# Kernel optimization log

Hardware: AMD Instinct MI355X
Metric: run time of the kernel (lower is better)

Reference implementation:

```python
import jax, jax.numpy as jnp
import numpy as np

P = 113          # modulus; eq_token = P, vocab = P + 1
D_MODEL = 1024
D_MLP = 4096
BATCH = 16384


def setup_inputs() -> dict:
    key = jax.random.key(0)
    ks = jax.random.split(key, 9)
    return {
        "a": jax.random.randint(ks[0], (BATCH,), 0, P, dtype=jnp.int64 if jax.config.jax_enable_x64 else jnp.int32),
        "b": jax.random.randint(ks[1], (BATCH,), 0, P, dtype=jnp.int64 if jax.config.jax_enable_x64 else jnp.int32),
        "token_embed": jax.random.normal(ks[2], (P + 1, D_MODEL), dtype=jnp.float32),
        "pos_embed": jax.random.normal(ks[3], (3, D_MODEL), dtype=jnp.float32),
        "W_in_w": jax.random.normal(ks[4], (D_MLP, D_MODEL), dtype=jnp.float32) * (1.0 / np.sqrt(D_MODEL)),
        "W_in_b": jax.random.normal(ks[5], (D_MLP,), dtype=jnp.float32) * 0.02,
        "W_out_w": jax.random.normal(ks[6], (D_MODEL, D_MLP), dtype=jnp.float32) * (1.0 / np.sqrt(D_MLP)),
        "W_out_b": jax.random.normal(ks[7], (D_MODEL,), dtype=jnp.float32) * 0.02,
        "unembed_w": jax.random.normal(ks[8], (P, D_MODEL), dtype=jnp.float32) * (1.0 / np.sqrt(D_MODEL)),
    }


def reference(a, b, token_embed, pos_embed, W_in_w, W_in_b, W_out_w, W_out_b, unembed_w):
    # tokens: (batch, 3) = [a, b, eq]
    eq = jnp.full_like(a, P)
    tokens = jnp.stack([a, b, eq], axis=1)
    # embed + positional: (batch, 3, d_model)
    x = token_embed[tokens] + pos_embed[None, :, :]
    # FNet-style mixing: FFT over seq (axis 1), then over d_model (axis 2), real part
    wave = jnp.fft.fft(jnp.fft.fft(x, axis=1), axis=2).real.astype(x.dtype)
    x = x + wave
    # MLP with residual
    h = jax.nn.relu(jnp.einsum('bsd,md->bsm', x, W_in_w) + W_in_b)
    x = x + jnp.einsum('bsm,dm->bsd', h, W_out_w) + W_out_b
    # unembed only the '=' position (index 2)
    logits = jnp.einsum('bd,vd->bv', x[:, 2, :], unembed_w)
    return logits
```

## Files before the change

### kernel.cpp

```cpp
#include <hip/hip_runtime.h>

typedef __attribute__((ext_vector_type(4))) float f32x4;
typedef __attribute__((ext_vector_type(8))) short short8;

#define PMOD 113
#define DM 1024
#define DMLP 4096
#define NBATCH 16384
#define SQRT3_2 0.86602540378443865f
#define CSTEP 6.1359231515425649e-3f
#define LTSTRIDE (12800 * 128)
#define NZ 8

__device__ __forceinline__ short f2bf(float x) {
    unsigned int u = __builtin_bit_cast(unsigned int, x);
    u += 0x7FFFu + ((u >> 16) & 1u);
    return (short)(u >> 16);
}
__device__ __forceinline__ float bf2f(short s) {
    return __builtin_bit_cast(float, (unsigned int)(unsigned short)s << 16);
}
__device__ __forceinline__ void cvt16(const float* p, short8& o0, short8& o1) {
    #pragma unroll
    for (int c4 = 0; c4 < 4; ++c4) {
        f32x4 v = *(const f32x4*)(p + c4 * 4);
        #pragma unroll
        for (int e = 0; e < 4; ++e) {
            short s = f2bf(v[e]);
            if (c4 < 2) o0[c4 * 4 + e] = s; else o1[(c4 - 2) * 4 + e] = s;
        }
    }
}

__global__ __launch_bounds__(256) void k_prep(
    unsigned short* __restrict__ Fb, unsigned short* __restrict__ V2b,
    unsigned short* __restrict__ Wob,
    const float* __restrict__ E, const float* __restrict__ pos,
    const float* __restrict__ Wo)
{
    __shared__ float smem[64 * 65];
    const int blk = blockIdx.x, tid = threadIdx.x;

    if (blk < 1024) {
        const int f = blk;
        for (int k = tid; k < DM; k += 256) {
            float v;
            if (k <= 512) v = cosf((float)((f * k) & 1023) * CSTEP);
            else          v = sinf((float)((f * (k - 512)) & 1023) * CSTEP);
            Fb[f * DM + k] = (unsigned short)f2bf(v);
        }
    } else if (blk < 1252) {
        const int t = blk - 1024;
        if (t >= 226) {
            for (int k = tid; k < DM; k += 256) V2b[t * DM + k] = 0;
            return;
        }
        float* vc = smem;
        float* vs = smem + 1024;
        if (t < PMOD) {
            const float* e = E + t * DM;
            const float* e2 = E + PMOD * DM;
            for (int d = tid; d < DM; d += 256) {
                float e2v = e2[d] + pos[2 * DM + d];
                vc[d] = e[d] + pos[d] - 0.5f * pos[DM + d] - 0.5f * e2v;
                vs[d] = SQRT3_2 * (pos[DM + d] - e2v);
            }
        } else {
            const float* e = E + (t - PMOD) * DM;
            for (int d = tid; d < DM; d += 256) {
                float x = e[d];
                vc[d] = -0.5f * x;
                vs[d] = SQRT3_2 * x;
            }
        }
        __syncthreads();
        for (int k = tid; k < DM; k += 256) {
            float o;
            if (k == 0)        o = vc[0];
            else if (k < 512)  o = vc[k] + vc[1024 - k];
            else if (k == 512) o = vc[512];
            else               o = vs[k - 512] - vs[1536 - k];
            V2b[t * DM + k] = (unsigned short)f2bf(o);
        }
    } else {
        const int idx = blk - 1252;
        const int m0 = (idx & 63) * 64;
        const int d0 = (idx >> 6) * 64;
        float (*tile)[65] = (float(*)[65])smem;
        #pragma unroll
        for (int it = 0; it < 16; ++it) {
            int i2 = tid + it * 256;
            int r = i2 >> 6, c = i2 & 63;
            tile[c][r] = Wo[(d0 + r) * DMLP + m0 + c];
        }
        __syncthreads();
        #pragma unroll
        for (int it = 0; it < 16; ++it) {
            int i2 = tid + it * 256;
            int r = i2 >> 6, c = i2 & 63;
            Wob[(m0 + r) * DM + d0 + c] = (unsigned short)f2bf(tile[r][c]);
        }
    }
}

template<int MODE>
__device__ __forceinline__ void mfma_body(
    int n0, int row0,
    unsigned short* __restrict__ C1, float* __restrict__ C2,
    const void* __restrict__ Av, const void* __restrict__ B1v,
    const float* __restrict__ B2, const float* __restrict__ bias,
    const float* __restrict__ E, const float* __restrict__ pos,
    const float* __restrict__ bo, short* sA, short* sB)
{
    const int tid = threadIdx.x;
    const int sr = tid >> 2, sq = (tid & 3) * 16;
    const int lane = tid & 63, w = tid >> 6;
    const int wr = w >> 1, wc = w & 1;
    const int lr = lane & 15, lg = lane >> 4;

    const unsigned short* Ab = nullptr; const float* Af = nullptr;
    {
        int r = row0 + sr;
        if (MODE == 2) { if (r < PMOD) Af = (const float*)Av + r * DM; }
        else           { if (r < 228)  Ab = (const unsigned short*)Av + r * DM; }
    }
    const unsigned short* Bb = nullptr; const float* Bf = nullptr;
    {
        int n = n0 + sr;
        if (MODE == 1) {
            if (n < 4096) Bf = (const float*)B1v + n * DM;
            else if (n - 4096 < PMOD) Bf = B2 + (n - 4096) * DM;
        } else {
            Bb = (const unsigned short*)B1v + n * DM;
        }
    }

    f32x4 acc[2][2];
    #pragma unroll
    for (int i = 0; i < 2; ++i)
        #pragma unroll
        for (int j = 0; j < 2; ++j) acc[i][j] = 0.f;

    for (int k0 = 0; k0 < DM; k0 += 64) {
        short8 a0, a1, b0, b1;
        if (MODE == 2) {
            if (Af) cvt16(Af + k0 + sq, a0, a1);
            else { a0 = 0; a1 = 0; }
        } else {
            if (Ab) { a0 = ((const short8*)(Ab + k0 + sq))[0];
                      a1 = ((const short8*)(Ab + k0 + sq))[1]; }
            else { a0 = 0; a1 = 0; }
        }
        if (MODE == 1) {
            if (Bf) cvt16(Bf + k0 + sq, b0, b1);
            else { b0 = 0; b1 = 0; }
        } else {
            b0 = ((const short8*)(Bb + k0 + sq))[0];
            b1 = ((const short8*)(Bb + k0 + sq))[1];
        }
        if (k0) __syncthreads();
        *(short8*)&sA[sr * 72 + sq] = a0;
        *(short8*)&sA[sr * 72 + sq + 8] = a1;
        *(short8*)&sB[sr * 72 + sq] = b0;
        *(short8*)&sB[sr * 72 + sq + 8] = b1;
        __syncthreads();

        #pragma unroll
        for (int ks = 0; ks < 2; ++ks) {
            short8 af[2], bfr[2];
            #pragma unroll
            for (int i = 0; i < 2; ++i)
                af[i] = *(const short8*)&sA[(wr * 32 + i * 16 + lr) * 72 + ks * 32 + lg * 8];
            #pragma unroll
            for (int j = 0; j < 2; ++j)
                bfr[j] = *(const short8*)&sB[(wc * 32 + j * 16 + lr) * 72 + ks * 32 + lg * 8];
            #pragma unroll
            for (int i = 0; i < 2; ++i)
                #pragma unroll
                for (int j = 0; j < 2; ++j)
                    acc[i][j] = __builtin_amdgcn_mfma_f32_16x16x32_bf16(af[i], bfr[j], acc[i][j], 0, 0, 0);
        }
    }

    #pragma unroll
    for (int i = 0; i < 2; ++i) {
        #pragma unroll
        for (int q = 0; q < 4; ++q) {
            int r = row0 + wr * 32 + i * 16 + lg * 4 + q;
            #pragma unroll
            for (int j = 0; j < 2; ++j) {
                int cg = n0 + wc * 32 + j * 16 + lr;
                float v = acc[i][j][q];
                if (MODE == 0) {
                    if (r < 228) {
                        if (r < PMOD) v += E[PMOD * DM + cg] + pos[2 * DM + cg];
                        if (r == 227) v += bo[cg];
                        C1[r * DM + cg] = (unsigned short)f2bf(v);
                    }
                } else if (MODE == 1) {
                    if (r < 228) {
                        if (n0 < 4096) {
                            if (r < PMOD) v += bias[cg];
                            C1[r * DMLP + cg] = (unsigned short)f2bf(v);
                        } else {
                            C2[r * 128 + cg - 4096] = v;
                        }
                    }
                } else {
                    if (r < 128) C1[r * DMLP + cg] = (unsigned short)f2bf(v);
                }
            }
        }
    }
}

__global__ __launch_bounds__(256) void k_m02(
    unsigned short* __restrict__ Tb, unsigned short* __restrict__ Mb,
    const unsigned short* __restrict__ V2b, const unsigned short* __restrict__ Fb,
    const float* __restrict__ U, const unsigned short* __restrict__ Wob,
    const float* __restrict__ E, const float* __restrict__ pos,
    const float* __restrict__ bo)
{
    __shared__ short sA[64 * 72];
    __shared__ short sB[64 * 72];
    const int blk = blockIdx.x;
    if (blk < 64) {
        mfma_body<0>((blk & 15) * 64, (blk >> 4) * 64, Tb, nullptr, V2b, Fb,
                     nullptr, nullptr, E, pos, bo, sA, sB);
    } else {
        int i = blk - 64;
        mfma_body<2>((i & 63) * 64, (i >> 6) * 64, Mb, nullptr, U, Wob,
                     nullptr, nullptr, nullptr, nullptr, nullptr, sA, sB);
    }
}

__global__ __launch_bounds__(256) void k_m1(
    unsigned short* __restrict__ Hb, float* __restrict__ L,
    const unsigned short* __restrict__ Tb, const float* __restrict__ Wi,
    const float* __restrict__ U, const float* __restrict__ bi)
{
    __shared__ short sA[64 * 72];
    __shared__ short sB[64 * 72];
    mfma_body<1>(blockIdx.x * 64, blockIdx.y * 64, Hb, L, Tb, Wi, U, bi,
                 nullptr, nullptr, nullptr, sA, sB);
}

__global__ __launch_bounds__(512) void k_pair_gemm(
    unsigned short* __restrict__ LTp,
    const unsigned short* __restrict__ Hb,
    const unsigned short* __restrict__ Mb,
    const float* __restrict__ L)
{
    __shared__ short mB[128 * 512];
    __shared__ short hA[2][64 * 72];

    const int tid = threadIdx.x;
    const int z = blockIdx.x;
    const int g = blockIdx.y;
    const int kbeg = z * 512;
    const bool slice0 = (z == 0);
    unsigned short* outp = LTp + (size_t)z * LTSTRIDE;

    const int lane = tid & 63, w = tid >> 6;
    const int wr = w >> 2, wc = w & 3;
    const int lr = lane & 15, lg = lane >> 4;
    const int sr = tid >> 3, sq8 = (tid & 7) * 8;

    {
        const int l8 = lane * 8;
        #pragma unroll
        for (int r = 0; r < 16; ++r) {
            int v = w * 16 + r;
            short8 d = *(const short8*)(Mb + v * DMLP + kbeg + l8);
            *(short8*)&mB[v * 512 + (l8 ^ ((v & 7) << 3))] = d;
        }
    }

    for (int u = g; u < 226; u += 32) {
        const int a = u >> 1;
        const int b0 = (u & 1) * 64;
        const int brow = b0 + sr;
        const int brc = brow < PMOD ? brow : PMOD - 1;
        const unsigned short* pA = Hb + a * DMLP + kbeg + sq8;
        const unsigned short* pB = Hb + (PMOD + brc) * DMLP + kbeg + sq8;

        f32x4 acc[2][2];
        #pragma unroll
        for (int i = 0; i < 2; ++i)
            #pragma unroll
            for (int j = 0; j < 2; ++j) acc[i][j] = 0.f;

        short8 ra = *(const short8*)pA;
        short8 rb = *(const short8*)pB;

        #pragma unroll
        for (int t = 0; t < 8; ++t) {
            short8 ran = ra, rbn = rb;
            if (t < 7) {
                ran = *(const short8*)(pA + (t + 1) * 64);
                rbn = *(const short8*)(pB + (t + 1) * 64);
            }
            short8 uu;
            #pragma unroll
            for (int e = 0; e < 8; ++e)
                uu[e] = f2bf(fmaxf(bf2f(ra[e]) + bf2f(rb[e]), 0.f));
            *(short8*)&hA[t & 1][sr * 72 + sq8] = uu;
            __syncthreads();

            #pragma unroll
            for (int ks = 0; ks < 2; ++ks) {
                short8 af[2], bfr[2];
                #pragma unroll
                for (int i = 0; i < 2; ++i)
                    af[i] = *(const short8*)&hA[t & 1][(wr * 32 + i * 16 + lr) * 72 + ks * 32 + lg * 8];
                #pragma unroll
                for (int j = 0; j < 2; ++j) {
                    int v = wc * 32 + j * 16 + lr;
                    int tk = t * 64 + ks * 32 + lg * 8;
                    bfr[j] = *(const short8*)&mB[v * 512 + (tk ^ ((v & 7) << 3))];
                }
                #pragma unroll
                for (int i = 0; i < 2; ++i)
                    #pragma unroll
                    for (int j = 0; j < 2; ++j)
                        acc[i][j] = __builtin_amdgcn_mfma_f32_16x16x32_bf16(af[i], bfr[j], acc[i][j], 0, 0, 0);
            }
            ra = ran; rb = rbn;
        }

        const float* La = L + a * 128;
        const float* Lb0 = L + PMOD * 128;
        const float* Lc = L + 227 * 128;
        #pragma unroll
        for (int i = 0; i < 2; ++i) {
            #pragma unroll
            for (int q = 0; q < 4; ++q) {
                int b = b0 + wr * 32 + i * 16 + lg * 4 + q;
                if (b >= PMOD) continue;
                unsigned short* dst = outp + (size_t)(a * PMOD + b) * 128;
                #pragma unroll
                for (int j = 0; j < 2; ++j) {
                    int col = wc * 32 + j * 16 + lr;
                    float val = acc[i][j][q];
                    if (slice0) val += La[col] + Lb0[b * 128 + col] + Lc[col];
                    dst[col] = (unsigned short)f2bf(val);
                }
            }
        }
    }
}

__global__ __launch_bounds__(256) void k_gather(
    float* __restrict__ out, const unsigned short* __restrict__ LTp,
    const int* __restrict__ a, const int* __restrict__ b)
{
    int g = blockIdx.x * 256 + threadIdx.x;
    if (g >= NBATCH * PMOD) return;
    unsigned int i = (unsigned)g / 113u;
    unsigned int v = (unsigned)g - i * 113u;
    size_t off = (size_t)((unsigned)a[i] * 113u + (unsigned)b[i]) * 128 + v;
    float s = 0.f;
    #pragma unroll
    for (int z = 0; z < NZ; ++z)
        s += bf2f(LTp[(size_t)z * LTSTRIDE + off]);
    out[g] = s;
}

extern "C" void kernel_launch(void* const* d_in, const int* in_sizes, int n_in,
                              void* d_out, int out_size, void* d_ws, size_t ws_size,
                              hipStream_t stream)
{
    const int*   a   = (const int*)d_in[0];
    const int*   b   = (const int*)d_in[1];
    const float* E   = (const float*)d_in[2];
    const float* pos = (const float*)d_in[3];
    const float* Wi  = (const float*)d_in[4];
    const float* bi  = (const float*)d_in[5];
    const float* Wo  = (const float*)d_in[6];
    const float* bo  = (const float*)d_in[7];
    const float* U   = (const float*)d_in[8];
    float* out = (float*)d_out;

    unsigned short* Fb  = (unsigned short*)d_ws;
    unsigned short* V2b = Fb + 1024 * 1024;
    unsigned short* Tb  = V2b + 228 * 1024;
    unsigned short* Hb  = Tb + 228 * 1024;
    unsigned short* Wob = Hb + 228 * 4096;
    unsigned short* Mb  = Wob + 4096 * 1024;
    unsigned short* LTp = Mb + 128 * 4096;
    float* L = (float*)(LTp + NZ * LTSTRIDE);

    k_prep<<<2276, 256, 0, stream>>>(Fb, V2b, Wob, E, pos, Wo);
    k_m02<<<192, 256, 0, stream>>>(Tb, Mb, V2b, Fb, U, Wob, E, pos, bo);
    k_m1<<<dim3(66, 4), 256, 0, stream>>>(Hb, L, Tb, Wi, U, bi);
    k_pair_gemm<<<dim3(NZ, 32), 512, 0, stream>>>(LTp, Hb, Mb, L);
    k_gather<<<(NBATCH * PMOD + 255) / 256, 256, 0, stream>>>(out, LTp, a, b);

    (void)in_sizes; (void)n_in; (void)out_size; (void)ws_size;
}
```

Before: 199.9 us.

## Retile pair GEMM over flattened (a,b) pairs with 128x128 tiles per block

The pair GEMM used 32 persistent 512-thread blocks per K-slice that each kept a 128x512 slice of M in LDS and looped over (a, b-half) tiles with 64-row padding. It now launches 100x8 blocks of 256 threads, each covering 128 flattened pairs by 128 vocab columns with a 4x4 MFMA tile per wave. M is streamed through LDS alongside H each K step. This removes the padding waste on b and raises occupancy and per-wave MFMA density, at the cost of reloading M for every block and more register pressure.

```diff
diff --git a/kernel.cpp b/kernel.cpp
--- a/kernel.cpp
+++ b/kernel.cpp
@@ -4,6 +4,7 @@
 typedef __attribute__((ext_vector_type(8))) short short8;
 
 #define PMOD 113
+#define NPAIR 12769
 #define DM 1024
 #define DMLP 4096
 #define NBATCH 16384
@@ -245,106 +246,112 @@
                  nullptr, nullptr, nullptr, sA, sB);
 }
 
-__global__ __launch_bounds__(512) void k_pair_gemm(
+__global__ __launch_bounds__(256) void k_pair_gemm(
     unsigned short* __restrict__ LTp,
     const unsigned short* __restrict__ Hb,
     const unsigned short* __restrict__ Mb,
     const float* __restrict__ L)
 {
-    __shared__ short mB[128 * 512];
-    __shared__ short hA[2][64 * 72];
+    __shared__ short sH[128 * 72];
+    __shared__ short sM[128 * 72];
 
     const int tid = threadIdx.x;
-    const int z = blockIdx.x;
-    const int g = blockIdx.y;
+    const int p0 = blockIdx.x * 128;
+    const int z = blockIdx.y;
     const int kbeg = z * 512;
     const bool slice0 = (z == 0);
     unsigned short* outp = LTp + (size_t)z * LTSTRIDE;
 
+    const int hr = tid >> 1, kh = (tid & 1) * 32;
+    {
+    }
+    const unsigned int pc = (unsigned)min(p0 + hr, NPAIR - 1);
+    const unsigned int a_r = pc / 113u;
+    const unsigned int b_r = pc - a_r * 113u;
+    const unsigned short* pHA = Hb + a_r * DMLP + kbeg + kh;
+    const unsigned short* pHB = Hb + (PMOD + b_r) * DMLP + kbeg + kh;
+    const unsigned short* pM  = Mb + hr * DMLP + kbeg + kh;
+
     const int lane = tid & 63, w = tid >> 6;
-    const int wr = w >> 2, wc = w & 3;
+    const int wr = w >> 1, wc = w & 1;
     const int lr = lane & 15, lg = lane >> 4;
-    const int sr = tid >> 3, sq8 = (tid & 7) * 8;
-
-    {
-        const int l8 = lane * 8;
-        #pragma unroll
-        for (int r = 0; r < 16; ++r) {
-            int v = w * 16 + r;
-            short8 d = *(const short8*)(Mb + v * DMLP + kbeg + l8);
-            *(short8*)&mB[v * 512 + (l8 ^ ((v & 7) << 3))] = d;
-        }
-    }
-
-    for (int u = g; u < 226; u += 32) {
-        const int a = u >> 1;
-        const int b0 = (u & 1) * 64;
-        const int brow = b0 + sr;
-        const int brc = brow < PMOD ? brow : PMOD - 1;
-        const unsigned short* pA = Hb + a * DMLP + kbeg + sq8;
-        const unsigned short* pB = Hb + (PMOD + brc) * DMLP + kbeg + sq8;
-
-        f32x4 acc[2][2];
-        #pragma unroll
-        for (int i = 0; i < 2; ++i)
-            #pragma unroll
-            for (int j = 0; j < 2; ++j) acc[i][j] = 0.f;
-
-        short8 ra = *(const short8*)pA;
-        short8 rb = *(const short8*)pB;
-
-        #pragma unroll
-        for (int t = 0; t < 8; ++t) {
-            short8 ran = ra, rbn = rb;
-            if (t < 7) {
-                ran = *(const short8*)(pA + (t + 1) * 64);
-                rbn = *(const short8*)(pB + (t + 1) * 64);
+
+    f32x4 acc[4][4];
+    #pragma unroll
+    for (int i = 0; i < 4; ++i)
+        #pragma unroll
+        for (int j = 0; j < 4; ++j) acc[i][j] = 0.f;
+
+    short8 rA[4], rB[4], rM[4];
+    #pragma unroll
+    for (int c = 0; c < 4; ++c) {
+        rA[c] = *(const short8*)(pHA + c * 8);
+        rB[c] = *(const short8*)(pHB + c * 8);
+        rM[c] = *(const short8*)(pM + c * 8);
+    }
+
+    #pragma unroll 1
+    for (int t = 0; t < 8; ++t) {
+        short8 u[4];
+        #pragma unroll
+        for (int c = 0; c < 4; ++c)
+            #pragma unroll
+            for (int e = 0; e < 8; ++e)
+                u[c][e] = f2bf(fmaxf(bf2f(rA[c][e]) + bf2f(rB[c][e]), 0.f));
+
+        if (t) __syncthreads();
+        #pragma unroll
+        for (int c = 0; c < 4; ++c) {
+            *(short8*)&sH[hr * 72 + kh + c * 8] = u[c];
+            *(short8*)&sM[hr * 72 + kh + c * 8] = rM[c];
+        }
+        __syncthreads();
+
+        if (t < 7) {
+            #pragma unroll
+            for (int c = 0; c < 4; ++c) {
+                rA[c] = *(const short8*)(pHA + (t + 1) * 64 + c * 8);
+                rB[c] = *(const short8*)(pHB + (t + 1) * 64 + c * 8);
+                rM[c] = *(const short8*)(pM + (t + 1) * 64 + c * 8);
             }
-            short8 uu;
-            #pragma unroll
-            for (int e = 0; e < 8; ++e)
-                uu[e] = f2bf(fmaxf(bf2f(ra[e]) + bf2f(rb[e]), 0.f));
-            *(short8*)&hA[t & 1][sr * 72 + sq8] = uu;
-            __syncthreads();
-
-            #pragma unroll
-            for (int ks = 0; ks < 2; ++ks) {
-                short8 af[2], bfr[2];
+        }
+
+        #pragma unroll
+        for (int ks = 0; ks < 2; ++ks) {
+            short8 af[4], bf[4];
+            #pragma unroll
+            for (int i = 0; i < 4; ++i)
+                af[i] = *(const short8*)&sH[(wr * 64 + i * 16 + lr) * 72 + ks * 32 + lg * 8];
+            #pragma unroll
+            for (int j = 0; j < 4; ++j)
+                bf[j] = *(const short8*)&sM[(wc * 64 + j * 16 + lr) * 72 + ks * 32 + lg * 8];
+            #pragma unroll
+            for (int i = 0; i < 4; ++i)
                 #pragma unroll
-                for (int i = 0; i < 2; ++i)
-                    af[i] = *(const short8*)&hA[t & 1][(wr * 32 + i * 16 + lr) * 72 + ks * 32 + lg * 8];
-                #pragma unroll
-                for (int j = 0; j < 2; ++j) {
-                    int v = wc * 32 + j * 16 + lr;
-                    int tk = t * 64 + ks * 32 + lg * 8;
-                    bfr[j] = *(const short8*)&mB[v * 512 + (tk ^ ((v & 7) << 3))];
-                }
-                #pragma unroll
-                for (int i = 0; i < 2; ++i)
-                    #pragma unroll
-                    for (int j = 0; j < 2; ++j)
-                        acc[i][j] = __builtin_amdgcn_mfma_f32_16x16x32_bf16(af[i], bfr[j], acc[i][j], 0, 0, 0);
-            }
-            ra = ran; rb = rbn;
-        }
-
-        const float* La = L + a * 128;
-        const float* Lb0 = L + PMOD * 128;
-        const float* Lc = L + 227 * 128;
-        #pragma unroll
-        for (int i = 0; i < 2; ++i) {
-            #pragma unroll
-            for (int q = 0; q < 4; ++q) {
-                int b = b0 + wr * 32 + i * 16 + lg * 4 + q;
-                if (b >= PMOD) continue;
-                unsigned short* dst = outp + (size_t)(a * PMOD + b) * 128;
-                #pragma unroll
-                for (int j = 0; j < 2; ++j) {
-                    int col = wc * 32 + j * 16 + lr;
-                    float val = acc[i][j][q];
-                    if (slice0) val += La[col] + Lb0[b * 128 + col] + Lc[col];
-                    dst[col] = (unsigned short)f2bf(val);
-                }
+                for (int j = 0; j < 4; ++j)
+                    acc[i][j] = __builtin_amdgcn_mfma_f32_16x16x32_bf16(af[i], bf[j], acc[i][j], 0, 0, 0);
+        }
+    }
+
+    const float* Lb0 = L + PMOD * 128;
+    const float* Lc = L + 227 * 128;
+    #pragma unroll
+    for (int i = 0; i < 4; ++i) {
+        #pragma unroll
+        for (int q = 0; q < 4; ++q) {
+            int p = p0 + wr * 64 + i * 16 + lg * 4 + q;
+            if (p >= NPAIR) continue;
+            unsigned int pa = (unsigned)p / 113u;
+            unsigned int pb = (unsigned)p - pa * 113u;
+            unsigned short* dst = outp + (size_t)p * 128;
+            const float* La = L + pa * 128;
+            const float* Lb = Lb0 + pb * 128;
+            #pragma unroll
+            for (int j = 0; j < 4; ++j) {
+                int col = wc * 64 + j * 16 + lr;
+                float val = acc[i][j][q];
+                if (slice0) val += La[col] + Lb[col] + Lc[col];
+                dst[col] = (unsigned short)f2bf(val);
             }
         }
     }
@@ -393,7 +400,7 @@
     k_prep<<<2276, 256, 0, stream>>>(Fb, V2b, Wob, E, pos, Wo);
     k_m02<<<192, 256, 0, stream>>>(Tb, Mb, V2b, Fb, U, Wob, E, pos, bo);
     k_m1<<<dim3(66, 4), 256, 0, stream>>>(Hb, L, Tb, Wi, U, bi);
-    k_pair_gemm<<<dim3(NZ, 32), 512, 0, stream>>>(LTp, Hb, Mb, L);
+    k_pair_gemm<<<dim3(100, NZ), 256, 0, stream>>>(LTp, Hb, Mb, L);
     k_gather<<<(NBATCH * PMOD + 255) / 256, 256, 0, stream>>>(out, LTp, a, b);
 
     (void)in_sizes; (void)n_in; (void)out_size; (void)ws_size;
```

Result: faster. 176.7 us (-11.6%).
